# Optimization experiments

Measured on AMD Instinct MI355X. Metric: run time of the kernel, lower is better.

Reference implementation:

```python
import jax, jax.numpy as jnp
import numpy as np

N = 50000        # num_electrodes / nodes
C = 32           # in_channels
H = 32           # hid_channels
K = 3            # num Chebyshev layers
E = 1_600_000    # num edges (avg degree 32)
FC_HID = 64      # fc1 hidden size
NUM_CLASSES = 2
BN_EPS = 1e-5


def setup_inputs() -> dict:
    key = jax.random.key(0)
    ks = jax.random.split(key, 10)
    x = jax.random.normal(ks[0], (N, C), dtype=jnp.float32)
    edge_index = jax.random.randint(ks[1], (2, E), 0, N, dtype=jnp.int64)
    edge_weight = jax.random.uniform(ks[2], (E,), dtype=jnp.float32)
    # per-layer GraphConvolution weights [K, C, H] (xavier-ish scale)
    W = jax.random.normal(ks[3], (K, C, H), dtype=jnp.float32) * (2.0 / (C + H)) ** 0.5
    # BatchNorm1d(in_channels) parameters (eval mode, running stats)
    bn_gamma = jnp.ones((C,), dtype=jnp.float32)
    bn_beta = jnp.zeros((C,), dtype=jnp.float32)
    bn_mean = jax.random.normal(ks[4], (C,), dtype=jnp.float32) * 0.01
    bn_var = jax.random.uniform(ks[5], (C,), dtype=jnp.float32) * 0.5 + 0.5
    # fc1: Linear(N*H -> FC_HID), fc2: Linear(FC_HID -> NUM_CLASSES)
    fc1_w = jax.random.normal(ks[6], (FC_HID, N * H), dtype=jnp.float32) * 1e-3
    fc1_b = jnp.zeros((FC_HID,), dtype=jnp.float32)
    fc2_w = jax.random.normal(ks[7], (NUM_CLASSES, FC_HID), dtype=jnp.float32) * 0.1
    fc2_b = jnp.zeros((NUM_CLASSES,), dtype=jnp.float32)
    return {
        "x": x, "edge_weight": edge_weight, "W": W,
        "bn_gamma": bn_gamma, "bn_beta": bn_beta, "bn_mean": bn_mean, "bn_var": bn_var,
        "fc1_w": fc1_w, "fc1_b": fc1_b, "fc2_w": fc2_w, "fc2_b": fc2_b,
        "edge_index": edge_index,
    }


def reference(x, edge_weight, W, bn_gamma, bn_beta, bn_mean, bn_var,
              fc1_w, fc1_b, fc2_w, fc2_b, edge_index):
    # BatchNorm1d over channels (eval mode): x is [N, C]
    x = (x - bn_mean) * jax.lax.rsqrt(bn_var + BN_EPS) * bn_gamma + bn_beta

    src, dst = edge_index[0], edge_index[1]
    self_loop = (src == dst)
    xj = x[src]  # gather source node features [E, C]

    # k == 0 term: edge weights replaced by self-loop indicator (T_0 identity term)
    w0 = jnp.where(self_loop, jnp.float32(1.0), jnp.float32(0.0))
    agg0 = jax.ops.segment_sum(w0[:, None] * xj, dst, num_segments=N)      # [N, C]
    # k >= 1 terms all share the same aggregated message (same edge_weight),
    # so aggregate once and contract with the summed weights W[1:]
    agg = jax.ops.segment_sum(edge_weight[:, None] * xj, dst, num_segments=N)  # [N, C]

    result = agg0 @ W[0] + agg @ W[1:].sum(axis=0)  # [N, H]
    result = jax.nn.relu(result).reshape(1, -1)     # [1, N*H]

    h = jax.nn.relu(result @ fc1_w.T + fc1_b)       # [1, FC_HID]
    out = h @ fc2_w.T + fc2_b                       # [1, NUM_CLASSES]
    return out
```

## Files before the change

### kernel.cpp

```cpp
#include <hip/hip_runtime.h>

constexpr int N_NODES = 50000;
constexpr int E_EDGES = 1600000;
constexpr int NH      = N_NODES * 32;
constexpr float BN_EPS = 1e-5f;
constexpr int NPAD    = 50016;
constexpr int NBLK    = 625;

__global__ void zero_kernel(float4* __restrict__ p, int n4) {
    int i = blockIdx.x * blockDim.x + threadIdx.x;
    if (i < n4) p[i] = make_float4(0.f, 0.f, 0.f, 0.f);
}

__global__ void hist_kernel(const int* __restrict__ ei, int* __restrict__ counts) {
    int e = blockIdx.x * blockDim.x + threadIdx.x;
    if (e < E_EDGES) atomicAdd(&counts[ei[E_EDGES + e]], 1);
}

__device__ inline int block_excl_scan(int v, int* s) {
    int t = threadIdx.x;
    s[t] = v;
    __syncthreads();
    for (int d = 1; d < 256; d <<= 1) {
        int x = (t >= d) ? s[t - d] : 0;
        __syncthreads();
        s[t] += x;
        __syncthreads();
    }
    return s[t] - v;
}

__global__ void scan1_kernel(const int* __restrict__ counts, int* __restrict__ bsum) {
    int i = blockIdx.x * 256 + threadIdx.x;
    int v = (i < N_NODES) ? counts[i] : 0;
#pragma unroll
    for (int o = 32; o > 0; o >>= 1) v += __shfl_down(v, o);
    __shared__ int s[4];
    int wave = threadIdx.x >> 6, lane = threadIdx.x & 63;
    if (lane == 0) s[wave] = v;
    __syncthreads();
    if (threadIdx.x == 0) bsum[blockIdx.x] = s[0] + s[1] + s[2] + s[3];
}

__global__ void scan2_kernel(int* __restrict__ bsum) {
    __shared__ int s[256];
    int t = threadIdx.x;
    int v = (t < 196) ? bsum[t] : 0;
    int excl = block_excl_scan(v, s);
    if (t < 196) bsum[t] = excl;
}

__global__ void scan3_kernel(const int* __restrict__ counts, const int* __restrict__ bsum,
                             int* __restrict__ off, int* __restrict__ cursor) {
    __shared__ int s[256];
    int i = blockIdx.x * 256 + threadIdx.x;
    int v = (i < N_NODES) ? counts[i] : 0;
    int excl = block_excl_scan(v, s) + bsum[blockIdx.x];
    if (i < N_NODES) { off[i] = excl; cursor[i] = excl; }
    if (i == N_NODES - 1) off[N_NODES] = excl + v;
}

__global__ void place_kernel(const int* __restrict__ ei, const float* __restrict__ ew,
                             int* __restrict__ cursor, int2* __restrict__ ep) {
    int e = blockIdx.x * blockDim.x + threadIdx.x;
    if (e < E_EDGES) {
        int src = ei[e];
        int dst = ei[E_EDGES + e];
        int pos = atomicAdd(&cursor[dst], 1);
        ep[pos] = make_int2(src | ((src == dst) ? 0x80000000 : 0),
                            __float_as_int(ew[e]));
    }
}

__global__ void gather_kernel(const float* __restrict__ x,
                              const float* __restrict__ gamma,
                              const float* __restrict__ beta,
                              const float* __restrict__ mean,
                              const float* __restrict__ var,
                              const int*   __restrict__ off,
                              const int2*  __restrict__ ep,
                              const float* __restrict__ W,
                              float* __restrict__ rres) {
    __shared__ float2 s_wp[1024];
    __shared__ float  s_ap[4][64];
    int tid = threadIdx.x;
    for (int idx = tid; idx < 1024; idx += 256)
        s_wp[idx] = make_float2(W[1024 + idx] + W[2048 + idx], W[idx]);
    __syncthreads();

    int lane  = tid & 63;
    int c     = lane & 31;
    int half  = lane >> 5;
    int wslot = tid >> 6;
    int wid   = (blockIdx.x << 2) + wslot;

    float sc = gamma[c] * rsqrtf(var[c] + BN_EPS);
    float sh = beta[c] - mean[c] * sc;

    const float2* ap2 = (const float2*)s_ap[wslot];

#pragma unroll
    for (int i = 0; i < 2; i++) {
        int n  = (wid << 1) + i;
        int e0 = off[n];
        int nb = off[n + 1] - e0;
        const int2* e2 = ep + e0;

        float acc = 0.f, acc0 = 0.f;
        int base = 0;
        for (; base + 8 <= nb; base += 8) {
#pragma unroll
            for (int k = 0; k < 4; k++) {
                int2 p = e2[base + (k << 1) + half];
                float vv = fmaf(x[(p.x & 0x7fffffff) * 32 + c], sc, sh);
                acc = fmaf(__int_as_float(p.y), vv, acc);
                if (p.x < 0) acc0 += vv;
            }
        }
        for (; base + 2 <= nb; base += 2) {
            int2 p = e2[base + half];
            float vv = fmaf(x[(p.x & 0x7fffffff) * 32 + c], sc, sh);
            acc = fmaf(__int_as_float(p.y), vv, acc);
            if (p.x < 0) acc0 += vv;
        }
        if (base < nb && half == 0) {
            int2 p = e2[base];
            float vv = fmaf(x[(p.x & 0x7fffffff) * 32 + c], sc, sh);
            acc = fmaf(__int_as_float(p.y), vv, acc);
            if (p.x < 0) acc0 += vv;
        }

        acc  += __shfl_xor(acc,  32);
        acc0 += __shfl_xor(acc0, 32);

        __builtin_amdgcn_wave_barrier();
        s_ap[wslot][(c << 1) | half] = half ? acc0 : acc;
        __threadfence_block();
        __builtin_amdgcn_wave_barrier();

        float r = 0.f;
        int ccb = half << 4;
#pragma unroll
        for (int t = 0; t < 16; t++) {
            int cc = ccb + t;
            float2 ap = ap2[cc];
            float2 wp = s_wp[cc * 32 + c];
            r = fmaf(ap.x, wp.x, r);
            r = fmaf(ap.y, wp.y, r);
        }
        r += __shfl_xor(r, 32);
        if (half == 0) rres[n * 32 + c] = fmaxf(r, 0.f);
        __builtin_amdgcn_wave_barrier();
    }
}

constexpr int CHUNK = 2560;
__global__ void fc1_kernel(const float* __restrict__ r,
                           const float* __restrict__ w,
                           float* __restrict__ partial) {
    __shared__ float4 s_r[640];
    int tid = threadIdx.x;
    size_t ib = (size_t)blockIdx.x * CHUNK;
    const float4* r4 = (const float4*)(r + ib);
    for (int i = tid; i < 640; i += 256) s_r[i] = r4[i];
    __syncthreads();

    int wave = tid >> 6, lane = tid & 63;
    int jbase = wave * 16;
    float* pout = partial + blockIdx.x * 64;
    for (int jj = 0; jj < 16; jj += 2) {
        const float4* wa = (const float4*)(w + (size_t)(jbase + jj    ) * NH + ib);
        const float4* wb = (const float4*)(w + (size_t)(jbase + jj + 1) * NH + ib);
        float a0 = 0.f, a1 = 0.f;
#pragma unroll
        for (int k = 0; k < 10; k++) {
            float4 rv = s_r[lane + k * 64];
            float4 x0 = wa[lane + k * 64];
            float4 x1 = wb[lane + k * 64];
            a0 = fmaf(rv.x, x0.x, a0); a0 = fmaf(rv.y, x0.y, a0);
            a0 = fmaf(rv.z, x0.z, a0); a0 = fmaf(rv.w, x0.w, a0);
            a1 = fmaf(rv.x, x1.x, a1); a1 = fmaf(rv.y, x1.y, a1);
            a1 = fmaf(rv.z, x1.z, a1); a1 = fmaf(rv.w, x1.w, a1);
        }
#pragma unroll
        for (int o = 32; o > 0; o >>= 1) {
            a0 += __shfl_down(a0, o);
            a1 += __shfl_down(a1, o);
        }
        if (lane == 0) {
            pout[jbase + jj    ] = a0;
            pout[jbase + jj + 1] = a1;
        }
    }
}

__global__ void reduce_head_kernel(const float* __restrict__ partial,
                                   const float* __restrict__ fc1_b,
                                   const float* __restrict__ fc2_w,
                                   const float* __restrict__ fc2_b,
                                   float* __restrict__ out) {
    __shared__ float red[1024];
    int t = threadIdx.x;
    int j = t & 63, s = t >> 6;
    float a = 0.f;
    for (int b = s; b < NBLK; b += 16) a += partial[b * 64 + j];
    red[t] = a;
    __syncthreads();
    if (s == 0) {
        float h = fc1_b[j];
#pragma unroll
        for (int q = 0; q < 16; q++) h += red[q * 64 + j];
        h = fmaxf(h, 0.f);
#pragma unroll
        for (int k = 0; k < 2; k++) {
            float p = h * fc2_w[k * 64 + j];
#pragma unroll
            for (int o = 32; o > 0; o >>= 1) p += __shfl_down(p, o);
            if (j == 0) out[k] = p + fc2_b[k];
        }
    }
}

extern "C" void kernel_launch(void* const* d_in, const int* in_sizes, int n_in,
                              void* d_out, int out_size, void* d_ws, size_t ws_size,
                              hipStream_t stream) {
    const float* x     = (const float*)d_in[0];
    const float* ew    = (const float*)d_in[1];
    const float* W     = (const float*)d_in[2];
    const float* gamma = (const float*)d_in[3];
    const float* beta  = (const float*)d_in[4];
    const float* mean  = (const float*)d_in[5];
    const float* var   = (const float*)d_in[6];
    const float* fc1_w = (const float*)d_in[7];
    const float* fc1_b = (const float*)d_in[8];
    const float* fc2_w = (const float*)d_in[9];
    const float* fc2_b = (const float*)d_in[10];
    const int*   ei    = (const int*)d_in[11];
    float* out = (float*)d_out;

    float* partial = (float*)d_ws;
    int*   counts  = (int*)d_ws + 40000;
    int*   off     = (int*)d_ws + 40000 + NPAD;
    int*   cursor  = (int*)d_ws + 40000 + 2 * NPAD;
    int*   bsum    = (int*)d_ws + 40000 + 3 * NPAD;
    int2*  ep      = (int2*)(bsum + 256);
    float* rres    = (float*)(ep + E_EDGES);
    (void)ws_size; (void)in_sizes; (void)n_in; (void)out_size;

    {
        int n4 = NPAD / 4;
        zero_kernel<<<(n4 + 255) / 256, 256, 0, stream>>>((float4*)counts, n4);
    }
    hist_kernel <<<(E_EDGES + 255) / 256, 256, 0, stream>>>(ei, counts);
    scan1_kernel<<<196, 256, 0, stream>>>(counts, bsum);
    scan2_kernel<<<1,   256, 0, stream>>>(bsum);
    scan3_kernel<<<196, 256, 0, stream>>>(counts, bsum, off, cursor);
    place_kernel<<<(E_EDGES + 255) / 256, 256, 0, stream>>>(ei, ew, cursor, ep);
    gather_kernel<<<N_NODES / 8, 256, 0, stream>>>(x, gamma, beta, mean, var,
                                                   off, ep, W, rres);
    fc1_kernel <<<NBLK, 256, 0, stream>>>(rres, fc1_w, partial);
    reduce_head_kernel<<<1, 1024, 0, stream>>>(partial, fc1_b, fc2_w, fc2_b, out);
}
```

Before: 816.2 us.

## Fuse fc1 into gather kernel, merge scan stages, vectorize edge kernels

Folds the fc1 matrix-vector product into the graph gather kernel. Each block now multiplies its node outputs directly against the matching fc1 weight slices and writes per-block partial sums, so the intermediate node-feature buffer is no longer written and re-read, and the large weight stream can overlap with the gather. It also merges the two final scan kernels into one that redundantly scans the block sums per block, and makes the histogram and placement kernels handle two edges per thread with vectorized loads. In exchange, fc1 weight loads become per-lane strided row reads rather than coalesced ones, and the final reduction has many more partials to sum in a single block.

New measurement: 923.5 us. +13.1%, slower.

```diff
diff --git a/kernel.cpp b/kernel.cpp
--- a/kernel.cpp
+++ b/kernel.cpp
@@ -5,7 +5,7 @@
 constexpr int NH      = N_NODES * 32;
 constexpr float BN_EPS = 1e-5f;
 constexpr int NPAD    = 50016;
-constexpr int NBLK    = 625;
+constexpr int GBLK    = N_NODES / 8;
 
 __global__ void zero_kernel(float4* __restrict__ p, int n4) {
     int i = blockIdx.x * blockDim.x + threadIdx.x;
@@ -13,8 +13,12 @@
 }
 
 __global__ void hist_kernel(const int* __restrict__ ei, int* __restrict__ counts) {
-    int e = blockIdx.x * blockDim.x + threadIdx.x;
-    if (e < E_EDGES) atomicAdd(&counts[ei[E_EDGES + e]], 1);
+    int t = blockIdx.x * blockDim.x + threadIdx.x;
+    if (t < E_EDGES / 2) {
+        int2 d = ((const int2*)(ei + E_EDGES))[t];
+        atomicAdd(&counts[d.x], 1);
+        atomicAdd(&counts[d.y], 1);
+    }
 }
 
 __device__ inline int block_excl_scan(int v, int* s) {
@@ -42,47 +46,53 @@
     if (threadIdx.x == 0) bsum[blockIdx.x] = s[0] + s[1] + s[2] + s[3];
 }
 
-__global__ void scan2_kernel(int* __restrict__ bsum) {
-    __shared__ int s[256];
+__global__ void scan23_kernel(const int* __restrict__ counts, const int* __restrict__ bsum,
+                              int* __restrict__ off, int* __restrict__ cursor) {
+    __shared__ int s[256], s2[256], sb[256];
     int t = threadIdx.x;
-    int v = (t < 196) ? bsum[t] : 0;
-    int excl = block_excl_scan(v, s);
-    if (t < 196) bsum[t] = excl;
-}
-
-__global__ void scan3_kernel(const int* __restrict__ counts, const int* __restrict__ bsum,
-                             int* __restrict__ off, int* __restrict__ cursor) {
-    __shared__ int s[256];
-    int i = blockIdx.x * 256 + threadIdx.x;
+    int bv = (t < 196) ? bsum[t] : 0;
+    int bexcl = block_excl_scan(bv, s2);
+    sb[t] = bexcl;
+    __syncthreads();
+    int blockoff = sb[blockIdx.x];
+
+    int i = blockIdx.x * 256 + t;
     int v = (i < N_NODES) ? counts[i] : 0;
-    int excl = block_excl_scan(v, s) + bsum[blockIdx.x];
+    int excl = block_excl_scan(v, s) + blockoff;
     if (i < N_NODES) { off[i] = excl; cursor[i] = excl; }
     if (i == N_NODES - 1) off[N_NODES] = excl + v;
 }
 
 __global__ void place_kernel(const int* __restrict__ ei, const float* __restrict__ ew,
                              int* __restrict__ cursor, int2* __restrict__ ep) {
-    int e = blockIdx.x * blockDim.x + threadIdx.x;
-    if (e < E_EDGES) {
-        int src = ei[e];
-        int dst = ei[E_EDGES + e];
-        int pos = atomicAdd(&cursor[dst], 1);
-        ep[pos] = make_int2(src | ((src == dst) ? 0x80000000 : 0),
-                            __float_as_int(ew[e]));
-    }
-}
-
-__global__ void gather_kernel(const float* __restrict__ x,
-                              const float* __restrict__ gamma,
-                              const float* __restrict__ beta,
-                              const float* __restrict__ mean,
-                              const float* __restrict__ var,
-                              const int*   __restrict__ off,
-                              const int2*  __restrict__ ep,
-                              const float* __restrict__ W,
-                              float* __restrict__ rres) {
+    int t = blockIdx.x * blockDim.x + threadIdx.x;
+    if (t < E_EDGES / 2) {
+        int2   sp = ((const int2*)ei)[t];
+        int2   dp = ((const int2*)(ei + E_EDGES))[t];
+        float2 wp = ((const float2*)ew)[t];
+        int pos0 = atomicAdd(&cursor[dp.x], 1);
+        ep[pos0] = make_int2(sp.x | ((sp.x == dp.x) ? 0x80000000 : 0),
+                             __float_as_int(wp.x));
+        int pos1 = atomicAdd(&cursor[dp.y], 1);
+        ep[pos1] = make_int2(sp.y | ((sp.y == dp.y) ? 0x80000000 : 0),
+                             __float_as_int(wp.y));
+    }
+}
+
+__global__ void gather_fc1_kernel(const float* __restrict__ x,
+                                  const float* __restrict__ gamma,
+                                  const float* __restrict__ beta,
+                                  const float* __restrict__ mean,
+                                  const float* __restrict__ var,
+                                  const int*   __restrict__ off,
+                                  const int2*  __restrict__ ep,
+                                  const float* __restrict__ W,
+                                  const float* __restrict__ fc1_w,
+                                  float* __restrict__ partial) {
     __shared__ float2 s_wp[1024];
     __shared__ float  s_ap[4][64];
+    __shared__ float4 s_rr[4][8];
+    __shared__ float  s_red[256];
     int tid = threadIdx.x;
     for (int idx = tid; idx < 1024; idx += 256)
         s_wp[idx] = make_float2(W[1024 + idx] + W[2048 + idx], W[idx]);
@@ -97,7 +107,9 @@
     float sc = gamma[c] * rsqrtf(var[c] + BN_EPS);
     float sh = beta[c] - mean[c] * sc;
 
-    const float2* ap2 = (const float2*)s_ap[wslot];
+    const float2* ap2  = (const float2*)s_ap[wslot];
+    const float*  wrow = fc1_w + (size_t)lane * NH;
+    float facc = 0.f;
 
 #pragma unroll
     for (int i = 0; i < 2; i++) {
@@ -149,49 +161,30 @@
             r = fmaf(ap.y, wp.y, r);
         }
         r += __shfl_xor(r, 32);
-        if (half == 0) rres[n * 32 + c] = fmaxf(r, 0.f);
-        __builtin_amdgcn_wave_barrier();
-    }
-}
-
-constexpr int CHUNK = 2560;
-__global__ void fc1_kernel(const float* __restrict__ r,
-                           const float* __restrict__ w,
-                           float* __restrict__ partial) {
-    __shared__ float4 s_r[640];
-    int tid = threadIdx.x;
-    size_t ib = (size_t)blockIdx.x * CHUNK;
-    const float4* r4 = (const float4*)(r + ib);
-    for (int i = tid; i < 640; i += 256) s_r[i] = r4[i];
-    __syncthreads();
-
-    int wave = tid >> 6, lane = tid & 63;
-    int jbase = wave * 16;
-    float* pout = partial + blockIdx.x * 64;
-    for (int jj = 0; jj < 16; jj += 2) {
-        const float4* wa = (const float4*)(w + (size_t)(jbase + jj    ) * NH + ib);
-        const float4* wb = (const float4*)(w + (size_t)(jbase + jj + 1) * NH + ib);
-        float a0 = 0.f, a1 = 0.f;
-#pragma unroll
-        for (int k = 0; k < 10; k++) {
-            float4 rv = s_r[lane + k * 64];
-            float4 x0 = wa[lane + k * 64];
-            float4 x1 = wb[lane + k * 64];
-            a0 = fmaf(rv.x, x0.x, a0); a0 = fmaf(rv.y, x0.y, a0);
-            a0 = fmaf(rv.z, x0.z, a0); a0 = fmaf(rv.w, x0.w, a0);
-            a1 = fmaf(rv.x, x1.x, a1); a1 = fmaf(rv.y, x1.y, a1);
-            a1 = fmaf(rv.z, x1.z, a1); a1 = fmaf(rv.w, x1.w, a1);
-        }
-#pragma unroll
-        for (int o = 32; o > 0; o >>= 1) {
-            a0 += __shfl_down(a0, o);
-            a1 += __shfl_down(a1, o);
-        }
-        if (lane == 0) {
-            pout[jbase + jj    ] = a0;
-            pout[jbase + jj + 1] = a1;
-        }
-    }
+
+        __builtin_amdgcn_wave_barrier();
+        if (half == 0) ((float*)s_rr[wslot])[c] = fmaxf(r, 0.f);
+        __threadfence_block();
+        __builtin_amdgcn_wave_barrier();
+
+        const float4* wp4 = (const float4*)(wrow + ((size_t)n << 5));
+#pragma unroll
+        for (int q = 0; q < 8; q++) {
+            float4 wv = wp4[q];
+            float4 rv = s_rr[wslot][q];
+            facc = fmaf(rv.x, wv.x, facc);
+            facc = fmaf(rv.y, wv.y, facc);
+            facc = fmaf(rv.z, wv.z, facc);
+            facc = fmaf(rv.w, wv.w, facc);
+        }
+        __builtin_amdgcn_wave_barrier();
+    }
+
+    s_red[(wslot << 6) + lane] = facc;
+    __syncthreads();
+    if (wslot == 0)
+        partial[blockIdx.x * 64 + lane] =
+            s_red[lane] + s_red[64 + lane] + s_red[128 + lane] + s_red[192 + lane];
 }
 
 __global__ void reduce_head_kernel(const float* __restrict__ partial,
@@ -203,7 +196,7 @@
     int t = threadIdx.x;
     int j = t & 63, s = t >> 6;
     float a = 0.f;
-    for (int b = s; b < NBLK; b += 16) a += partial[b * 64 + j];
+    for (int b = s; b < GBLK; b += 16) a += partial[b * 64 + j];
     red[t] = a;
     __syncthreads();
     if (s == 0) {
@@ -239,25 +232,22 @@
     float* out = (float*)d_out;
 
     float* partial = (float*)d_ws;
-    int*   counts  = (int*)d_ws + 40000;
-    int*   off     = (int*)d_ws + 40000 + NPAD;
-    int*   cursor  = (int*)d_ws + 40000 + 2 * NPAD;
-    int*   bsum    = (int*)d_ws + 40000 + 3 * NPAD;
+    int*   counts  = (int*)d_ws + GBLK * 64;
+    int*   off     = counts + NPAD;
+    int*   cursor  = off + NPAD;
+    int*   bsum    = cursor + NPAD;
     int2*  ep      = (int2*)(bsum + 256);
-    float* rres    = (float*)(ep + E_EDGES);
     (void)ws_size; (void)in_sizes; (void)n_in; (void)out_size;
 
     {
         int n4 = NPAD / 4;
         zero_kernel<<<(n4 + 255) / 256, 256, 0, stream>>>((float4*)counts, n4);
     }
-    hist_kernel <<<(E_EDGES + 255) / 256, 256, 0, stream>>>(ei, counts);
-    scan1_kernel<<<196, 256, 0, stream>>>(counts, bsum);
-    scan2_kernel<<<1,   256, 0, stream>>>(bsum);
-    scan3_kernel<<<196, 256, 0, stream>>>(counts, bsum, off, cursor);
-    place_kernel<<<(E_EDGES + 255) / 256, 256, 0, stream>>>(ei, ew, cursor, ep);
-    gather_kernel<<<N_NODES / 8, 256, 0, stream>>>(x, gamma, beta, mean, var,
-                                                   off, ep, W, rres);
-    fc1_kernel <<<NBLK, 256, 0, stream>>>(rres, fc1_w, partial);
+    hist_kernel  <<<(E_EDGES / 2 + 255) / 256, 256, 0, stream>>>(ei, counts);
+    scan1_kernel <<<196, 256, 0, stream>>>(counts, bsum);
+    scan23_kernel<<<196, 256, 0, stream>>>(counts, bsum, off, cursor);
+    place_kernel <<<(E_EDGES / 2 + 255) / 256, 256, 0, stream>>>(ei, ew, cursor, ep);
+    gather_fc1_kernel<<<GBLK, 256, 0, stream>>>(x, gamma, beta, mean, var,
+                                                off, ep, W, fc1_w, partial);
     reduce_head_kernel<<<1, 1024, 0, stream>>>(partial, fc1_b, fc2_w, fc2_b, out);
 }
```

## Replace CSR sort-and-gather with atomic edge scatter; fuse node transform into fc1

Applied to the files above, without the earlier changes.

Drops the histogram/scan/placement pipeline that built a destination-sorted edge list. Each edge instead atomically adds its weighted normalized source features into a per-node aggregate, and self-loops are counted separately. The per-node W contraction and ReLU are fused into the fc1 kernel so intermediate node results stay in shared memory. This trades several passes and the sorted-edge buffer for tens of millions of contended float atomics and nondeterministic summation order.

Result: faster. 745.3 us (-8.7%).

```diff
diff --git a/kernel.cpp b/kernel.cpp
--- a/kernel.cpp
+++ b/kernel.cpp
@@ -4,176 +4,108 @@
 constexpr int E_EDGES = 1600000;
 constexpr int NH      = N_NODES * 32;
 constexpr float BN_EPS = 1e-5f;
-constexpr int NPAD    = 50016;
-constexpr int NBLK    = 625;
+constexpr int NBLK    = 1250;
+constexpr int CNT_PAD = 50016;
 
 __global__ void zero_kernel(float4* __restrict__ p, int n4) {
     int i = blockIdx.x * blockDim.x + threadIdx.x;
     if (i < n4) p[i] = make_float4(0.f, 0.f, 0.f, 0.f);
 }
 
-__global__ void hist_kernel(const int* __restrict__ ei, int* __restrict__ counts) {
-    int e = blockIdx.x * blockDim.x + threadIdx.x;
-    if (e < E_EDGES) atomicAdd(&counts[ei[E_EDGES + e]], 1);
-}
+__global__ void scatter_kernel(const float* __restrict__ x,
+                               const float* __restrict__ gamma,
+                               const float* __restrict__ beta,
+                               const float* __restrict__ mean,
+                               const float* __restrict__ var,
+                               const int*   __restrict__ ei,
+                               const float* __restrict__ ew,
+                               float* __restrict__ agg,
+                               int*   __restrict__ cnt_self) {
+    int tid  = threadIdx.x;
+    int lane = tid & 63;
+    int c    = lane & 31;
+    int half = lane >> 5;
+    int wid  = (blockIdx.x << 2) + (tid >> 6);
 
-__device__ inline int block_excl_scan(int v, int* s) {
-    int t = threadIdx.x;
-    s[t] = v;
-    __syncthreads();
-    for (int d = 1; d < 256; d <<= 1) {
-        int x = (t >= d) ? s[t - d] : 0;
-        __syncthreads();
-        s[t] += x;
-        __syncthreads();
-    }
-    return s[t] - v;
-}
+    float sc = gamma[c] * rsqrtf(var[c] + BN_EPS);
+    float sh = beta[c] - mean[c] * sc;
 
-__global__ void scan1_kernel(const int* __restrict__ counts, int* __restrict__ bsum) {
-    int i = blockIdx.x * 256 + threadIdx.x;
-    int v = (i < N_NODES) ? counts[i] : 0;
+    int ebase = __builtin_amdgcn_readfirstlane(wid << 5);
+    const int2*   sp = (const int2*)(ei + ebase);
+    const int2*   dp = (const int2*)(ei + E_EDGES + ebase);
+    const float2* wp = (const float2*)(ew + ebase);
+
 #pragma unroll
-    for (int o = 32; o > 0; o >>= 1) v += __shfl_down(v, o);
-    __shared__ int s[4];
-    int wave = threadIdx.x >> 6, lane = threadIdx.x & 63;
-    if (lane == 0) s[wave] = v;
-    __syncthreads();
-    if (threadIdx.x == 0) bsum[blockIdx.x] = s[0] + s[1] + s[2] + s[3];
-}
-
-__global__ void scan2_kernel(int* __restrict__ bsum) {
-    __shared__ int s[256];
-    int t = threadIdx.x;
-    int v = (t < 196) ? bsum[t] : 0;
-    int excl = block_excl_scan(v, s);
-    if (t < 196) bsum[t] = excl;
-}
-
-__global__ void scan3_kernel(const int* __restrict__ counts, const int* __restrict__ bsum,
-                             int* __restrict__ off, int* __restrict__ cursor) {
-    __shared__ int s[256];
-    int i = blockIdx.x * 256 + threadIdx.x;
-    int v = (i < N_NODES) ? counts[i] : 0;
-    int excl = block_excl_scan(v, s) + bsum[blockIdx.x];
-    if (i < N_NODES) { off[i] = excl; cursor[i] = excl; }
-    if (i == N_NODES - 1) off[N_NODES] = excl + v;
-}
-
-__global__ void place_kernel(const int* __restrict__ ei, const float* __restrict__ ew,
-                             int* __restrict__ cursor, int2* __restrict__ ep) {
-    int e = blockIdx.x * blockDim.x + threadIdx.x;
-    if (e < E_EDGES) {
-        int src = ei[e];
-        int dst = ei[E_EDGES + e];
-        int pos = atomicAdd(&cursor[dst], 1);
-        ep[pos] = make_int2(src | ((src == dst) ? 0x80000000 : 0),
-                            __float_as_int(ew[e]));
+    for (int k = 0; k < 16; k++) {
+        int2   s2 = sp[k];
+        int2   d2 = dp[k];
+        float2 w2 = wp[k];
+        int   src = half ? s2.y : s2.x;
+        int   dst = half ? d2.y : d2.x;
+        float w   = half ? w2.y : w2.x;
+        float vv  = fmaf(x[src * 32 + c], sc, sh);
+        atomicAdd(&agg[dst * 32 + c], w * vv);
+        if (src == dst && c == 0) atomicAdd(&cnt_self[dst], 1);
     }
 }
 
-__global__ void gather_kernel(const float* __restrict__ x,
-                              const float* __restrict__ gamma,
-                              const float* __restrict__ beta,
-                              const float* __restrict__ mean,
-                              const float* __restrict__ var,
-                              const int*   __restrict__ off,
-                              const int2*  __restrict__ ep,
-                              const float* __restrict__ W,
-                              float* __restrict__ rres) {
+__global__ void cfc1_kernel(const float* __restrict__ x,
+                            const float* __restrict__ gamma,
+                            const float* __restrict__ beta,
+                            const float* __restrict__ mean,
+                            const float* __restrict__ var,
+                            const float* __restrict__ agg,
+                            const int*   __restrict__ cnt_self,
+                            const float* __restrict__ W,
+                            const float* __restrict__ fc1_w,
+                            float* __restrict__ partial) {
     __shared__ float2 s_wp[1024];
-    __shared__ float  s_ap[4][64];
+    __shared__ float2 s_a[4][2][32];
+    __shared__ float4 s_r[320];
     int tid = threadIdx.x;
     for (int idx = tid; idx < 1024; idx += 256)
         s_wp[idx] = make_float2(W[1024 + idx] + W[2048 + idx], W[idx]);
     __syncthreads();
 
-    int lane  = tid & 63;
-    int c     = lane & 31;
-    int half  = lane >> 5;
-    int wslot = tid >> 6;
-    int wid   = (blockIdx.x << 2) + wslot;
-
+    int lane = tid & 63, c = lane & 31, half = lane >> 5, wslot = tid >> 6;
     float sc = gamma[c] * rsqrtf(var[c] + BN_EPS);
     float sh = beta[c] - mean[c] * sc;
-
-    const float2* ap2 = (const float2*)s_ap[wslot];
+    int   nb0 = blockIdx.x * 40 + wslot * 10;
+    float* s_rf = (float*)s_r;
 
 #pragma unroll
-    for (int i = 0; i < 2; i++) {
-        int n  = (wid << 1) + i;
-        int e0 = off[n];
-        int nb = off[n + 1] - e0;
-        const int2* e2 = ep + e0;
-
-        float acc = 0.f, acc0 = 0.f;
-        int base = 0;
-        for (; base + 8 <= nb; base += 8) {
-#pragma unroll
-            for (int k = 0; k < 4; k++) {
-                int2 p = e2[base + (k << 1) + half];
-                float vv = fmaf(x[(p.x & 0x7fffffff) * 32 + c], sc, sh);
-                acc = fmaf(__int_as_float(p.y), vv, acc);
-                if (p.x < 0) acc0 += vv;
-            }
-        }
-        for (; base + 2 <= nb; base += 2) {
-            int2 p = e2[base + half];
-            float vv = fmaf(x[(p.x & 0x7fffffff) * 32 + c], sc, sh);
-            acc = fmaf(__int_as_float(p.y), vv, acc);
-            if (p.x < 0) acc0 += vv;
-        }
-        if (base < nb && half == 0) {
-            int2 p = e2[base];
-            float vv = fmaf(x[(p.x & 0x7fffffff) * 32 + c], sc, sh);
-            acc = fmaf(__int_as_float(p.y), vv, acc);
-            if (p.x < 0) acc0 += vv;
-        }
-
-        acc  += __shfl_xor(acc,  32);
-        acc0 += __shfl_xor(acc0, 32);
-
+    for (int i = 0; i < 5; i++) {
+        int n = nb0 + 2 * i + half;
+        float a  = agg[n * 32 + c];
+        int   cs = cnt_self[n];
+        float a0 = cs ? (float)cs * fmaf(x[n * 32 + c], sc, sh) : 0.f;
         __builtin_amdgcn_wave_barrier();
-        s_ap[wslot][(c << 1) | half] = half ? acc0 : acc;
+        s_a[wslot][half][c] = make_float2(a, a0);
         __threadfence_block();
         __builtin_amdgcn_wave_barrier();
-
         float r = 0.f;
-        int ccb = half << 4;
 #pragma unroll
-        for (int t = 0; t < 16; t++) {
-            int cc = ccb + t;
-            float2 ap = ap2[cc];
-            float2 wp = s_wp[cc * 32 + c];
-            r = fmaf(ap.x, wp.x, r);
-            r = fmaf(ap.y, wp.y, r);
+        for (int cc = 0; cc < 32; cc++) {
+            float2 ap = s_a[wslot][half][cc];
+            float2 wv = s_wp[cc * 32 + c];
+            r = fmaf(ap.x, wv.x, r);
+            r = fmaf(ap.y, wv.y, r);
         }
-        r += __shfl_xor(r, 32);
-        if (half == 0) rres[n * 32 + c] = fmaxf(r, 0.f);
+        s_rf[(wslot * 10 + 2 * i + half) * 32 + c] = fmaxf(r, 0.f);
         __builtin_amdgcn_wave_barrier();
     }
-}
-
-constexpr int CHUNK = 2560;
-__global__ void fc1_kernel(const float* __restrict__ r,
-                           const float* __restrict__ w,
-                           float* __restrict__ partial) {
-    __shared__ float4 s_r[640];
-    int tid = threadIdx.x;
-    size_t ib = (size_t)blockIdx.x * CHUNK;
-    const float4* r4 = (const float4*)(r + ib);
-    for (int i = tid; i < 640; i += 256) s_r[i] = r4[i];
     __syncthreads();
 
-    int wave = tid >> 6, lane = tid & 63;
+    int wave = tid >> 6;
+    size_t ib = (size_t)blockIdx.x * 1280;
     int jbase = wave * 16;
     float* pout = partial + blockIdx.x * 64;
     for (int jj = 0; jj < 16; jj += 2) {
-        const float4* wa = (const float4*)(w + (size_t)(jbase + jj    ) * NH + ib);
-        const float4* wb = (const float4*)(w + (size_t)(jbase + jj + 1) * NH + ib);
+        const float4* wa = (const float4*)(fc1_w + (size_t)(jbase + jj    ) * NH + ib);
+        const float4* wb = (const float4*)(fc1_w + (size_t)(jbase + jj + 1) * NH + ib);
         float a0 = 0.f, a1 = 0.f;
 #pragma unroll
-        for (int k = 0; k < 10; k++) {
+        for (int k = 0; k < 5; k++) {
             float4 rv = s_r[lane + k * 64];
             float4 x0 = wa[lane + k * 64];
             float4 x1 = wb[lane + k * 64];
@@ -238,26 +170,18 @@
     const int*   ei    = (const int*)d_in[11];
     float* out = (float*)d_out;
 
-    float* partial = (float*)d_ws;
-    int*   counts  = (int*)d_ws + 40000;
-    int*   off     = (int*)d_ws + 40000 + NPAD;
-    int*   cursor  = (int*)d_ws + 40000 + 2 * NPAD;
-    int*   bsum    = (int*)d_ws + 40000 + 3 * NPAD;
-    int2*  ep      = (int2*)(bsum + 256);
-    float* rres    = (float*)(ep + E_EDGES);
+    float* agg      = (float*)d_ws;
+    int*   cnt_self = (int*)d_ws + NH;
+    float* partial  = (float*)d_ws + NH + CNT_PAD;
     (void)ws_size; (void)in_sizes; (void)n_in; (void)out_size;
 
     {
-        int n4 = NPAD / 4;
-        zero_kernel<<<(n4 + 255) / 256, 256, 0, stream>>>((float4*)counts, n4);
+        int n4 = (NH + CNT_PAD) / 4;
+        zero_kernel<<<(n4 + 255) / 256, 256, 0, stream>>>((float4*)d_ws, n4);
     }
-    hist_kernel <<<(E_EDGES + 255) / 256, 256, 0, stream>>>(ei, counts);
-    scan1_kernel<<<196, 256, 0, stream>>>(counts, bsum);
-    scan2_kernel<<<1,   256, 0, stream>>>(bsum);
-    scan3_kernel<<<196, 256, 0, stream>>>(counts, bsum, off, cursor);
-    place_kernel<<<(E_EDGES + 255) / 256, 256, 0, stream>>>(ei, ew, cursor, ep);
-    gather_kernel<<<N_NODES / 8, 256, 0, stream>>>(x, gamma, beta, mean, var,
-                                                   off, ep, W, rres);
-    fc1_kernel <<<NBLK, 256, 0, stream>>>(rres, fc1_w, partial);
+    scatter_kernel<<<12500, 256, 0, stream>>>(x, gamma, beta, mean, var,
+                                              ei, ew, agg, cnt_self);
+    cfc1_kernel<<<NBLK, 256, 0, stream>>>(x, gamma, beta, mean, var,
+                                          agg, cnt_self, W, fc1_w, partial);
     reduce_head_kernel<<<1, 1024, 0, stream>>>(partial, fc1_b, fc2_w, fc2_b, out);
 }
```
